# Kernel tuning notes

Measured on AMD Instinct MI355X. Metric: run time of the kernel, lower is better.

The kernel has to match this reference:

```python
import jax, jax.numpy as jnp
import numpy as np

EPS = 1e-8


def setup_inputs() -> dict:
    key = jax.random.key(0)
    ks = jax.random.split(key, 6)
    B, Cin, Cout, K, S, G = 8, 64, 64, 3, 512, 48
    fan_in = Cin * K * K * K
    bound_w = np.sqrt(6.0 / ((1 + 0.25 ** 2) * fan_in))  # kaiming_uniform a=0.25
    bound_b = 1.0 / np.sqrt(fan_in)
    bound_lin = 1.0 / np.sqrt(S)
    return {
        "x": jax.random.normal(ks[0], (B, Cin, G, G, G), jnp.float32),
        "style": jax.random.normal(ks[1], (B, S), jnp.float32),
        "weight": jax.random.uniform(ks[2], (Cout, Cin, K, K, K), jnp.float32, -bound_w, bound_w),
        "bias": jax.random.uniform(ks[3], (1, Cout, 1, 1, 1), jnp.float32, -bound_b, bound_b),
        "style_w": jax.random.uniform(ks[4], (Cin, S), jnp.float32, -bound_lin, bound_lin),
        "style_b": jax.random.uniform(ks[5], (Cin,), jnp.float32, -bound_lin, bound_lin),
    }


def reference(x, style, weight, bias, style_w, style_b):
    B, Cin = x.shape[0], x.shape[1]
    Cout, K = weight.shape[0], weight.shape[2]
    # style modulation scale per (sample, input channel)
    s = style @ style_w.T + style_b                      # [B, Cin]
    # modulate: per-sample weights [B, Cout, Cin, K, K, K]
    w = weight[None] * s[:, None, :, None, None, None]
    # demodulate: rsqrt of per-(sample, out-channel) variance
    var = jnp.sum(w * w, axis=(2, 3, 4, 5), keepdims=True)
    w = w * jax.lax.rsqrt(var + EPS)
    # grouped conv: merge batch into channels, groups = batch_size
    w = w.reshape(B * Cout, Cin, K, K, K)
    xg = x.reshape(1, B * Cin, *x.shape[2:])
    y = jax.lax.conv_general_dilated(
        xg, w,
        window_strides=(1, 1, 1),
        padding='VALID',
        dimension_numbers=('NCDHW', 'OIDHW', 'NCDHW'),
        feature_group_count=B,
    )
    y = y.reshape(B, Cout, *y.shape[2:])
    return y + bias
```

## Files before the change

kernel.cpp:

```cpp
#include <hip/hip_runtime.h>


typedef __bf16 bf16x8 __attribute__((ext_vector_type(8)));
typedef float  f32x4  __attribute__((ext_vector_type(4)));

static constexpr int   B_   = 8;
static constexpr int   S_   = 512;
static constexpr int   G_   = 48;
static constexpr int   O_   = 46;
static constexpr int   TAPS = 27;
static constexpr int   SPI  = G_ * G_ * G_;
static constexpr int   SPO  = O_ * O_ * O_;
static constexpr float EPSV = 1e-8f;

static constexpr size_t XT_OFF   = 0;
static constexpr size_t XT_BYTES = (size_t)B_ * SPI * 64 * 2;
static constexpr size_t WQ_OFF   = XT_OFF + XT_BYTES;
static constexpr size_t WQ_BYTES = (size_t)B_ * 2 * TAPS * 64 * 32 * 2;
static constexpr size_t S_OFF    = WQ_OFF + WQ_BYTES;
static constexpr size_t D_OFF    = S_OFF + 2048;

__device__ __forceinline__ unsigned short f2bf(float f) {
    unsigned int u = __float_as_uint(f);
    u = (u + 0x7fffu + ((u >> 16) & 1u)) >> 16;
    return (unsigned short)u;
}

__global__ void s_kernel(const float* __restrict__ style,
                         const float* __restrict__ style_w,
                         const float* __restrict__ style_b,
                         float* __restrict__ s_out)
{
    const int bg = blockIdx.x, b = bg >> 6, g = bg & 63, l = threadIdx.x;
    const float4* sp = (const float4*)(style + b * S_);
    const float4* wp = (const float4*)(style_w + g * S_);
    const float4 a0 = sp[l * 2], a1 = sp[l * 2 + 1];
    const float4 b0 = wp[l * 2], b1 = wp[l * 2 + 1];
    float acc = a0.x * b0.x + a0.y * b0.y + a0.z * b0.z + a0.w * b0.w
              + a1.x * b1.x + a1.y * b1.y + a1.z * b1.z + a1.w * b1.w;
#pragma unroll
    for (int m = 1; m <= 32; m <<= 1) acc += __shfl_xor(acc, m);
    if (l == 0) s_out[bg] = acc + style_b[g];
}

__global__ void d_kernel(const float* __restrict__ weight,
                         const float* __restrict__ s,
                         float* __restrict__ d_out)
{
    const int bc = blockIdx.x, b = bc >> 6, co = bc & 63, ci = threadIdx.x;
    const float sv = s[b * 64 + ci];
    const float* wp = weight + (co * 64 + ci) * TAPS;
    float v = 0.f;
#pragma unroll
    for (int i = 0; i < TAPS; ++i) { const float t = wp[i] * sv; v += t * t; }
#pragma unroll
    for (int m = 1; m <= 32; m <<= 1) v += __shfl_xor(v, m);
    if (ci == 0) d_out[bc] = rsqrtf(v + EPSV);
}

__global__ void wq_kernel(const float* __restrict__ weight,
                          const float* __restrict__ s,
                          const float* __restrict__ d,
                          unsigned short* __restrict__ wq)
{
    const int blk = blockIdx.x;
    const int b = blk / 27, tap = blk - b * 27;
    const int t = threadIdx.x;
#pragma unroll
    for (int it = 0; it < 2; ++it) {
        const int item = t + it * 256;
        const int kc = item >> 8;
        const int g  = (item >> 6) & 3;
        const int l  = item & 63;
        const int co = g * 16 + (l & 15);
        const int ci0 = kc * 32 + ((l >> 4) * 8);
        const float dd = d[b * 64 + co];
        unsigned int u[4];
#pragma unroll
        for (int k = 0; k < 4; ++k) {
            const int ci = ci0 + 2 * k;
            const float w0 = weight[(co * 64 + ci)     * TAPS + tap] * s[b * 64 + ci]     * dd;
            const float w1 = weight[(co * 64 + ci + 1) * TAPS + tap] * s[b * 64 + ci + 1] * dd;
            u[k] = (unsigned)f2bf(w0) | ((unsigned)f2bf(w1) << 16);
        }
        uint4 v; v.x = u[0]; v.y = u[1]; v.z = u[2]; v.w = u[3];
        *(uint4*)(wq + ((size_t)((b * 2 + kc) * 27 + tap)) * 2048 + (g * 64 + l) * 8) = v;
    }
}

__global__ void xT_kernel(const float* __restrict__ x,
                          unsigned short* __restrict__ xT)
{
    const int blk = blockIdx.x;
    const int b = blk / 1728;
    const int sp0 = (blk - b * 1728) * 64;
    const int t = threadIdx.x;
    __shared__ float tile[64][65];

    const int cr = t >> 4;
    const int s4 = (t & 15) * 4;
#pragma unroll
    for (int r = 0; r < 4; ++r) {
        const int ci = r * 16 + cr;
        const float4 v = *(const float4*)(x + ((size_t)b * 64 + ci) * SPI + sp0 + s4);
        tile[ci][s4]     = v.x;
        tile[ci][s4 + 1] = v.y;
        tile[ci][s4 + 2] = v.z;
        tile[ci][s4 + 3] = v.w;
    }
    __syncthreads();

    const int ci8 = (t & 7) * 8;
    const int spq = t >> 3;
#pragma unroll
    for (int p = 0; p < 2; ++p) {
        const int sp = spq + 32 * p;
        unsigned int u[4];
#pragma unroll
        for (int k = 0; k < 4; ++k) {
            const unsigned int lo = f2bf(tile[ci8 + 2 * k][sp]);
            const unsigned int hi = f2bf(tile[ci8 + 2 * k + 1][sp]);
            u[k] = lo | (hi << 16);
        }
        uint4 v; v.x = u[0]; v.y = u[1]; v.z = u[2]; v.w = u[3];
        *(uint4*)(xT + ((size_t)b * SPI + sp0 + sp) * 64 + ci8) = v;
    }
}

#define XST     80
#define XTILE_B (648 * 80)

__global__ __launch_bounds__(256, 3) void conv_kernel(
    const unsigned short* __restrict__ xT,
    const unsigned short* __restrict__ wq,
    const float* __restrict__ bias,
    float* __restrict__ out)
{
    __shared__ __align__(16) char xs[XTILE_B];

    const int t = threadIdx.x;
    const int p  = blockIdx.x;
    const int lg = (p & 7) * 432 + (p >> 3);
    const int xt = lg % 3;
    const int r0 = lg / 3;
    const int yt = r0 % 12;
    const int bz = r0 / 12;
    const int b  = bz / 12, zt = bz - b * 12;
    const int x0 = xt * 16;
    const int y0 = (yt < 11) ? yt * 4 : 42;
    const int z0 = (zt < 11) ? zt * 4 : 42;

    const unsigned short* const xb = xT + (size_t)b * (SPI * 64);
    const unsigned short* const wb = wq + (size_t)b * (2 * TAPS * 2048);

    const int w = t >> 6, l = t & 63, kg = l >> 4, l16 = l & 15;
    const int ch = w & 1, zp = w >> 1;
    const unsigned short* const wa = wb + ch * 1024 + l * 8;
    const int bbase = (zp * 216 + l16) * XST + kg * 16;
    constexpr int FOFF[8] = {0, 1440, 2880, 4320, 8640, 10080, 11520, 12960};

    f32x4 acc[16];
#pragma unroll
    for (int i = 0; i < 16; ++i) acc[i] = (f32x4){0.f, 0.f, 0.f, 0.f};

    auto x_src = [&](int i, int kc) -> const uint4* {
        const int sp = i >> 2, cg = i & 3;
        const int iz = sp / 108;
        const int r1 = sp - iz * 108;
        const int iy = r1 / 18;
        const int ix = r1 - iy * 18;
        int gx = x0 + ix; if (gx > 47) gx = 47;
        return (const uint4*)(xb +
            ((((z0 + iz) * 48) + (y0 + iy)) * 48 + gx) * 64 + kc * 32 + cg * 8);
    };

#pragma unroll
    for (int j = 0; j < 10; ++j) {
        const int i = t + j * 256;
        const uint4 v = *x_src(i, 0);
        *(uint4*)(xs + (i >> 2) * XST + (i & 3) * 16) = v;
    }
    if (t < 32) {
        const int i = 2560 + t;
        const uint4 v = *x_src(i, 0);
        *(uint4*)(xs + (i >> 2) * XST + (i & 3) * 16) = v;
    }

    bf16x8 a0 = *(const bf16x8*)(wa);
    bf16x8 a1 = *(const bf16x8*)(wa + 512);

    __syncthreads();

    uint4 pv[10];
#pragma unroll
    for (int j = 0; j < 10; ++j)
        pv[j] = *x_src(t + j * 256, 1);

    auto tap_body = [&](int kt, int ktn) {
        const bf16x8 n0 = *(const bf16x8*)(wa + (size_t)ktn * 2048);
        const bf16x8 n1 = *(const bf16x8*)(wa + (size_t)ktn * 2048 + 512);
        const int tap = (kt >= 27) ? kt - 27 : kt;
        const int kz = tap / 9;
        const int r2 = tap - kz * 9;
        const int ky = r2 / 3;
        const int kx = r2 - ky * 3;
        const int toff = (kz * 108 + ky * 18 + kx) * XST;
#pragma unroll
        for (int nf = 0; nf < 8; ++nf) {
            const bf16x8 bv = *(const bf16x8*)(xs + toff + bbase + FOFF[nf]);
            acc[nf]     = __builtin_amdgcn_mfma_f32_16x16x32_bf16(a0, bv, acc[nf],     0, 0, 0);
            acc[8 + nf] = __builtin_amdgcn_mfma_f32_16x16x32_bf16(a1, bv, acc[8 + nf], 0, 0, 0);
        }
        a0 = n0; a1 = n1;
    };

#pragma unroll 1
    for (int kt = 0; kt < 27; ++kt)
        tap_body(kt, kt + 1);

    __syncthreads();
#pragma unroll
    for (int j = 0; j < 10; ++j) {
        const int i = t + j * 256;
        *(uint4*)(xs + (i >> 2) * XST + (i & 3) * 16) = pv[j];
    }
    if (t < 32) {
        const int i = 2560 + t;
        const uint4 v = *x_src(i, 1);
        *(uint4*)(xs + (i >> 2) * XST + (i & 3) * 16) = v;
    }
    __syncthreads();

#pragma unroll 1
    for (int kt = 27; kt < 54; ++kt)
        tap_body(kt, (kt + 1 < 54) ? kt + 1 : 53);

    const size_t ob = (size_t)b * 64 * SPO;
    const int ox = x0 + l16;
    if (ox < O_) {
#pragma unroll
        for (int cf = 0; cf < 2; ++cf) {
#pragma unroll
            for (int nf = 0; nf < 8; ++nf) {
                const int oz = z0 + 2 * zp + (nf >> 2);
                const int oy = y0 + (nf & 3);
                const f32x4 v = acc[cf * 8 + nf];
                const size_t so = (size_t)oz * 2116 + oy * 46 + ox;
#pragma unroll
                for (int r = 0; r < 4; ++r) {
                    const int co = ch * 32 + cf * 16 + kg * 4 + r;
                    out[ob + (size_t)co * SPO + so] = v[r] + bias[co];
                }
            }
        }
    }
}

extern "C" void kernel_launch(void* const* d_in, const int* in_sizes, int n_in,
                              void* d_out, int out_size, void* d_ws, size_t ws_size,
                              hipStream_t stream)
{
    const float* x       = (const float*)d_in[0];
    const float* style   = (const float*)d_in[1];
    const float* weight  = (const float*)d_in[2];
    const float* bias    = (const float*)d_in[3];
    const float* style_w = (const float*)d_in[4];
    const float* style_b = (const float*)d_in[5];
    float* out = (float*)d_out;

    char* ws = (char*)d_ws;
    unsigned short* xT  = (unsigned short*)(ws + XT_OFF);
    unsigned short* wqp = (unsigned short*)(ws + WQ_OFF);
    float* sbuf = (float*)(ws + S_OFF);
    float* dbuf = (float*)(ws + D_OFF);

    hipLaunchKernelGGL(s_kernel, dim3(512), dim3(64), 0, stream,
                       style, style_w, style_b, sbuf);
    hipLaunchKernelGGL(d_kernel, dim3(512), dim3(64), 0, stream,
                       weight, sbuf, dbuf);
    hipLaunchKernelGGL(wq_kernel, dim3(216), dim3(256), 0, stream,
                       weight, sbuf, dbuf, wqp);
    hipLaunchKernelGGL(xT_kernel, dim3(B_ * (SPI / 64)), dim3(256), 0, stream,
                       x, xT);
    hipLaunchKernelGGL(conv_kernel, dim3(3456), dim3(256), 0, stream,
                       xT, wqp, bias, out);
}
```

Measured before the change: 606.4 us.

## Fuse weight prep kernels and restructure conv MFMA tiling with double-buffered operands

Merges the style, demodulation and weight-quantization kernels into one per-batch prep kernel that keeps s and d in shared memory, removing two launches. The conv kernel changes its warp tiling so each wave covers all 64 output channels for one z-plane. Its main loop double-buffers both A (weights) and B (LDS activations) fragments across taps and raises wave priority around MFMA bursts. The prefetch of the second channel half into registers is dropped in favor of a sync-and-reload. The prep kernel now runs on only 8 blocks, which may serialize that stage.

```diff
diff --git a/kernel.cpp b/kernel.cpp
--- a/kernel.cpp
+++ b/kernel.cpp
@@ -16,9 +16,6 @@
 static constexpr size_t XT_OFF   = 0;
 static constexpr size_t XT_BYTES = (size_t)B_ * SPI * 64 * 2;
 static constexpr size_t WQ_OFF   = XT_OFF + XT_BYTES;
-static constexpr size_t WQ_BYTES = (size_t)B_ * 2 * TAPS * 64 * 32 * 2;
-static constexpr size_t S_OFF    = WQ_OFF + WQ_BYTES;
-static constexpr size_t D_OFF    = S_OFF + 2048;
 
 __device__ __forceinline__ unsigned short f2bf(float f) {
     unsigned int u = __float_as_uint(f);
@@ -26,47 +23,51 @@
     return (unsigned short)u;
 }
 
-__global__ void s_kernel(const float* __restrict__ style,
-                         const float* __restrict__ style_w,
-                         const float* __restrict__ style_b,
-                         float* __restrict__ s_out)
+__global__ __launch_bounds__(256) void prep_kernel(
+    const float* __restrict__ style,
+    const float* __restrict__ style_w,
+    const float* __restrict__ style_b,
+    const float* __restrict__ weight,
+    unsigned short* __restrict__ wq)
 {
-    const int bg = blockIdx.x, b = bg >> 6, g = bg & 63, l = threadIdx.x;
-    const float4* sp = (const float4*)(style + b * S_);
-    const float4* wp = (const float4*)(style_w + g * S_);
-    const float4 a0 = sp[l * 2], a1 = sp[l * 2 + 1];
-    const float4 b0 = wp[l * 2], b1 = wp[l * 2 + 1];
-    float acc = a0.x * b0.x + a0.y * b0.y + a0.z * b0.z + a0.w * b0.w
-              + a1.x * b1.x + a1.y * b1.y + a1.z * b1.z + a1.w * b1.w;
-#pragma unroll
-    for (int m = 1; m <= 32; m <<= 1) acc += __shfl_xor(acc, m);
-    if (l == 0) s_out[bg] = acc + style_b[g];
-}
-
-__global__ void d_kernel(const float* __restrict__ weight,
-                         const float* __restrict__ s,
-                         float* __restrict__ d_out)
-{
-    const int bc = blockIdx.x, b = bc >> 6, co = bc & 63, ci = threadIdx.x;
-    const float sv = s[b * 64 + ci];
-    const float* wp = weight + (co * 64 + ci) * TAPS;
-    float v = 0.f;
-#pragma unroll
-    for (int i = 0; i < TAPS; ++i) { const float t = wp[i] * sv; v += t * t; }
-#pragma unroll
-    for (int m = 1; m <= 32; m <<= 1) v += __shfl_xor(v, m);
-    if (ci == 0) d_out[bc] = rsqrtf(v + EPSV);
-}
-
-__global__ void wq_kernel(const float* __restrict__ weight,
-                          const float* __restrict__ s,
-                          const float* __restrict__ d,
-                          unsigned short* __restrict__ wq)
-{
-    const int blk = blockIdx.x;
-    const int b = blk / 27, tap = blk - b * 27;
-    const int t = threadIdx.x;
-#pragma unroll
+    __shared__ float s_sh[64];
+    __shared__ float d_sh[64];
+    const int b = blockIdx.x, t = threadIdx.x;
+
+    {
+        const int g = t >> 2, q = t & 3;
+        const float4* sp = (const float4*)(style + b * S_) + q * 32;
+        const float4* wp = (const float4*)(style_w + g * S_) + q * 32;
+        float acc = 0.f;
+#pragma unroll
+        for (int i = 0; i < 32; ++i) {
+            const float4 a = sp[i], w4 = wp[i];
+            acc += a.x * w4.x + a.y * w4.y + a.z * w4.z + a.w * w4.w;
+        }
+        acc += __shfl_xor(acc, 1);
+        acc += __shfl_xor(acc, 2);
+        if (q == 0) s_sh[g] = acc + style_b[g];
+    }
+    __syncthreads();
+
+    {
+        const int co = t >> 2, q = t & 3;
+        float v = 0.f;
+#pragma unroll 1
+        for (int j = 0; j < 16; ++j) {
+            const int ci = q * 16 + j;
+            const float sv = s_sh[ci];
+            const float* wp = weight + (co * 64 + ci) * TAPS;
+#pragma unroll
+            for (int i = 0; i < TAPS; ++i) { const float x = wp[i] * sv; v += x * x; }
+        }
+        v += __shfl_xor(v, 1);
+        v += __shfl_xor(v, 2);
+        if (q == 0) d_sh[co] = rsqrtf(v + EPSV);
+    }
+    __syncthreads();
+
+#pragma unroll 1
     for (int it = 0; it < 2; ++it) {
         const int item = t + it * 256;
         const int kc = item >> 8;
@@ -74,17 +75,20 @@
         const int l  = item & 63;
         const int co = g * 16 + (l & 15);
         const int ci0 = kc * 32 + ((l >> 4) * 8);
-        const float dd = d[b * 64 + co];
-        unsigned int u[4];
-#pragma unroll
-        for (int k = 0; k < 4; ++k) {
-            const int ci = ci0 + 2 * k;
-            const float w0 = weight[(co * 64 + ci)     * TAPS + tap] * s[b * 64 + ci]     * dd;
-            const float w1 = weight[(co * 64 + ci + 1) * TAPS + tap] * s[b * 64 + ci + 1] * dd;
-            u[k] = (unsigned)f2bf(w0) | ((unsigned)f2bf(w1) << 16);
-        }
-        uint4 v; v.x = u[0]; v.y = u[1]; v.z = u[2]; v.w = u[3];
-        *(uint4*)(wq + ((size_t)((b * 2 + kc) * 27 + tap)) * 2048 + (g * 64 + l) * 8) = v;
+        const float dd = d_sh[co];
+#pragma unroll 1
+        for (int tap = 0; tap < TAPS; ++tap) {
+            unsigned int u[4];
+#pragma unroll
+            for (int k = 0; k < 4; ++k) {
+                const int ci = ci0 + 2 * k;
+                const float w0 = weight[(co * 64 + ci)     * TAPS + tap] * s_sh[ci]     * dd;
+                const float w1 = weight[(co * 64 + ci + 1) * TAPS + tap] * s_sh[ci + 1] * dd;
+                u[k] = (unsigned)f2bf(w0) | ((unsigned)f2bf(w1) << 16);
+            }
+            uint4 v; v.x = u[0]; v.y = u[1]; v.z = u[2]; v.w = u[3];
+            *(uint4*)(wq + ((size_t)((b * 2 + kc) * 27 + tap)) * 2048 + (g * 64 + l) * 8) = v;
+        }
     }
 }
 
@@ -129,6 +133,19 @@
 
 #define XST     80
 #define XTILE_B (648 * 80)
+
+#define MFMA16(AS, BS)                                                        \
+    do {                                                                      \
+        __builtin_amdgcn_s_setprio(1);                                        \
+        _Pragma("unroll")                                                     \
+        for (int g_ = 0; g_ < 4; ++g_) {                                      \
+            _Pragma("unroll")                                                 \
+            for (int n_ = 0; n_ < 4; ++n_)                                    \
+                acc[g_ * 4 + n_] = __builtin_amdgcn_mfma_f32_16x16x32_bf16(   \
+                    AS[g_], BS[n_], acc[g_ * 4 + n_], 0, 0, 0);               \
+        }                                                                     \
+        __builtin_amdgcn_s_setprio(0);                                        \
+    } while (0)
 
 __global__ __launch_bounds__(256, 3) void conv_kernel(
     const unsigned short* __restrict__ xT,
@@ -154,14 +171,14 @@
     const unsigned short* const wb = wq + (size_t)b * (2 * TAPS * 2048);
 
     const int w = t >> 6, l = t & 63, kg = l >> 4, l16 = l & 15;
-    const int ch = w & 1, zp = w >> 1;
-    const unsigned short* const wa = wb + ch * 1024 + l * 8;
-    const int bbase = (zp * 216 + l16) * XST + kg * 16;
-    constexpr int FOFF[8] = {0, 1440, 2880, 4320, 8640, 10080, 11520, 12960};
+    const unsigned short* const wa = wb + l * 8;
+    const int bbase = (w * 108 + l16) * XST + kg * 16;
 
     f32x4 acc[16];
 #pragma unroll
     for (int i = 0; i < 16; ++i) acc[i] = (f32x4){0.f, 0.f, 0.f, 0.f};
+
+    bf16x8 aA[4], aB[4], bA[4], bB[4];
 
     auto x_src = [&](int i, int kc) -> const uint4* {
         const int sp = i >> 2, cg = i & 3;
@@ -174,81 +191,85 @@
             ((((z0 + iz) * 48) + (y0 + iy)) * 48 + gx) * 64 + kc * 32 + cg * 8);
     };
 
-#pragma unroll
-    for (int j = 0; j < 10; ++j) {
-        const int i = t + j * 256;
-        const uint4 v = *x_src(i, 0);
-        *(uint4*)(xs + (i >> 2) * XST + (i & 3) * 16) = v;
-    }
-    if (t < 32) {
-        const int i = 2560 + t;
-        const uint4 v = *x_src(i, 0);
-        *(uint4*)(xs + (i >> 2) * XST + (i & 3) * 16) = v;
-    }
-
-    bf16x8 a0 = *(const bf16x8*)(wa);
-    bf16x8 a1 = *(const bf16x8*)(wa + 512);
-
-    __syncthreads();
-
-    uint4 pv[10];
-#pragma unroll
-    for (int j = 0; j < 10; ++j)
-        pv[j] = *x_src(t + j * 256, 1);
-
-    auto tap_body = [&](int kt, int ktn) {
-        const bf16x8 n0 = *(const bf16x8*)(wa + (size_t)ktn * 2048);
-        const bf16x8 n1 = *(const bf16x8*)(wa + (size_t)ktn * 2048 + 512);
-        const int tap = (kt >= 27) ? kt - 27 : kt;
-        const int kz = tap / 9;
-        const int r2 = tap - kz * 9;
-        const int ky = r2 / 3;
-        const int kx = r2 - ky * 3;
-        const int toff = (kz * 108 + ky * 18 + kx) * XST;
-#pragma unroll
-        for (int nf = 0; nf < 8; ++nf) {
-            const bf16x8 bv = *(const bf16x8*)(xs + toff + bbase + FOFF[nf]);
-            acc[nf]     = __builtin_amdgcn_mfma_f32_16x16x32_bf16(a0, bv, acc[nf],     0, 0, 0);
-            acc[8 + nf] = __builtin_amdgcn_mfma_f32_16x16x32_bf16(a1, bv, acc[8 + nf], 0, 0, 0);
-        }
-        a0 = n0; a1 = n1;
-    };
-
-#pragma unroll 1
-    for (int kt = 0; kt < 27; ++kt)
-        tap_body(kt, kt + 1);
-
-    __syncthreads();
-#pragma unroll
-    for (int j = 0; j < 10; ++j) {
-        const int i = t + j * 256;
-        *(uint4*)(xs + (i >> 2) * XST + (i & 3) * 16) = pv[j];
-    }
-    if (t < 32) {
-        const int i = 2560 + t;
-        const uint4 v = *x_src(i, 1);
-        *(uint4*)(xs + (i >> 2) * XST + (i & 3) * 16) = v;
-    }
-    __syncthreads();
-
-#pragma unroll 1
-    for (int kt = 27; kt < 54; ++kt)
-        tap_body(kt, (kt + 1 < 54) ? kt + 1 : 53);
+#pragma unroll 1
+    for (int kc = 0; kc < 2; ++kc) {
+        const int base = kc * TAPS;
+
+#pragma unroll
+        for (int g = 0; g < 4; ++g) {
+            aA[g] = *(const bf16x8*)(wa + (size_t)(base    ) * 2048 + g * 512);
+            aB[g] = *(const bf16x8*)(wa + (size_t)(base + 1) * 2048 + g * 512);
+        }
+
+        if (kc) __syncthreads();
+
+#pragma unroll
+        for (int j = 0; j < 10; ++j) {
+            const int i = t + j * 256;
+            const uint4 v = *x_src(i, kc);
+            *(uint4*)(xs + (i >> 2) * XST + (i & 3) * 16) = v;
+        }
+        if (t < 32) {
+            const int i = 2560 + t;
+            const uint4 v = *x_src(i, kc);
+            *(uint4*)(xs + (i >> 2) * XST + (i & 3) * 16) = v;
+        }
+        __syncthreads();
+
+#pragma unroll
+        for (int nf = 0; nf < 4; ++nf)
+            bA[nf] = *(const bf16x8*)(xs + bbase + nf * (18 * XST));
+
+#pragma unroll 1
+        for (int j = 0; j < 13; ++j) {
+            const int t0 = 2 * j;
+            {
+                const int tb = t0 + 1;
+                const int kz = tb / 9, rr = tb - kz * 9;
+                const int ky = rr / 3, kx = rr - ky * 3;
+                const int toff = (kz * 108 + ky * 18 + kx) * XST;
+#pragma unroll
+                for (int nf = 0; nf < 4; ++nf)
+                    bB[nf] = *(const bf16x8*)(xs + toff + bbase + nf * (18 * XST));
+                MFMA16(aA, bA);
+                const size_t ao = (size_t)(base + t0 + 2) * 2048;
+#pragma unroll
+                for (int g = 0; g < 4; ++g)
+                    aA[g] = *(const bf16x8*)(wa + ao + g * 512);
+            }
+            {
+                const int tb = t0 + 2;
+                const int kz = tb / 9, rr = tb - kz * 9;
+                const int ky = rr / 3, kx = rr - ky * 3;
+                const int toff = (kz * 108 + ky * 18 + kx) * XST;
+#pragma unroll
+                for (int nf = 0; nf < 4; ++nf)
+                    bA[nf] = *(const bf16x8*)(xs + toff + bbase + nf * (18 * XST));
+                MFMA16(aB, bB);
+                int ta = base + t0 + 3; if (ta > 53) ta = 53;
+                const size_t ao = (size_t)ta * 2048;
+#pragma unroll
+                for (int g = 0; g < 4; ++g)
+                    aB[g] = *(const bf16x8*)(wa + ao + g * 512);
+            }
+        }
+        MFMA16(aA, bA);
+    }
 
     const size_t ob = (size_t)b * 64 * SPO;
+    const int oz = z0 + w;
     const int ox = x0 + l16;
     if (ox < O_) {
 #pragma unroll
-        for (int cf = 0; cf < 2; ++cf) {
-#pragma unroll
-            for (int nf = 0; nf < 8; ++nf) {
-                const int oz = z0 + 2 * zp + (nf >> 2);
-                const int oy = y0 + (nf & 3);
-                const f32x4 v = acc[cf * 8 + nf];
+        for (int g = 0; g < 4; ++g) {
+#pragma unroll
+            for (int nt = 0; nt < 4; ++nt) {
+                const int oy = y0 + nt;
+                const f32x4 v = acc[g * 4 + nt];
                 const size_t so = (size_t)oz * 2116 + oy * 46 + ox;
 #pragma unroll
                 for (int r = 0; r < 4; ++r) {
-                    const int co = ch * 32 + cf * 16 + kg * 4 + r;
+                    const int co = g * 16 + kg * 4 + r;
                     out[ob + (size_t)co * SPO + so] = v[r] + bias[co];
                 }
             }
@@ -271,15 +292,9 @@
     char* ws = (char*)d_ws;
     unsigned short* xT  = (unsigned short*)(ws + XT_OFF);
     unsigned short* wqp = (unsigned short*)(ws + WQ_OFF);
-    float* sbuf = (float*)(ws + S_OFF);
-    float* dbuf = (float*)(ws + D_OFF);
-
-    hipLaunchKernelGGL(s_kernel, dim3(512), dim3(64), 0, stream,
-                       style, style_w, style_b, sbuf);
-    hipLaunchKernelGGL(d_kernel, dim3(512), dim3(64), 0, stream,
-                       weight, sbuf, dbuf);
-    hipLaunchKernelGGL(wq_kernel, dim3(216), dim3(256), 0, stream,
-                       weight, sbuf, dbuf, wqp);
+
+    hipLaunchKernelGGL(prep_kernel, dim3(B_), dim3(256), 0, stream,
+                       style, style_w, style_b, weight, wqp);
     hipLaunchKernelGGL(xT_kernel, dim3(B_ * (SPI / 64)), dim3(256), 0, stream,
                        x, xT);
     hipLaunchKernelGGL(conv_kernel, dim3(3456), dim3(256), 0, stream,
```

Measured after the change: 619.4 us. 2.1% more time.
